# Kernel optimization log

Measured on AMD Instinct MI355X. Metric: run time of the kernel, lower is better.

Reference implementation:

```python
import jax, jax.numpy as jnp
import numpy as np

NEG_SLOPE = 0.2
N, IN_DIM, OUT_DIM, N_HEADS = 4096, 512, 512, 4
D_K = OUT_DIM // N_HEADS


def setup_inputs() -> dict:
    key = jax.random.key(0)
    k1, k2, k3, k4, k5 = jax.random.split(key, 5)
    H = jax.random.normal(k1, (N, IN_DIM), dtype=jnp.float32)
    A = jax.random.randint(k2, (N, N), 0, 2, dtype=jnp.int32)
    W = jax.random.normal(k3, (IN_DIM, OUT_DIM), dtype=jnp.float32) * (1.0 / np.sqrt(IN_DIM))
    a_l = jax.random.normal(k4, (N_HEADS, D_K), dtype=jnp.float32) * 0.1
    a_r = jax.random.normal(k5, (N_HEADS, D_K), dtype=jnp.float32) * 0.1
    return {"H": H, "A": A, "W": W, "a_l": a_l, "a_r": a_r}


def reference(H, A, W, a_l, a_r):
    n = H.shape[0]
    # mask = (A + I) > 0, shape (N, N); self-loops always allowed
    mask = (A + jnp.eye(n, dtype=A.dtype)) > 0
    # Wh: (N, heads, d_k)
    Wh = (H @ W).reshape(n, N_HEADS, D_K)
    sl = jnp.einsum('nhd,hd->nh', Wh, a_l)  # (N, heads)
    sr = jnp.einsum('nhd,hd->nh', Wh, a_r)  # (N, heads)
    # e[i, h, j] = leaky_relu(sl[i,h] + sr[j,h])
    e = jax.nn.leaky_relu(sl[:, :, None] + sr.T[None, :, :], negative_slope=NEG_SLOPE)
    e = jnp.where(mask[:, None, :], e, -jnp.inf)
    alpha = jnp.nan_to_num(jax.nn.softmax(e, axis=2), nan=0.0)  # dropout is identity at eval
    # out[i, h, :] = sum_j alpha[i,h,j] * Wh[j,h,:]
    out = jnp.einsum('nhm,mhd->nhd', alpha, Wh).reshape(n, OUT_DIM)
    return jax.nn.elu(out)
```

## Files before the change

### kernel.cpp

```cpp
#include <hip/hip_runtime.h>

typedef unsigned short ushort_t;
typedef __attribute__((ext_vector_type(8)))  short  short8;
typedef __attribute__((ext_vector_type(4)))  short  short4v;
typedef __attribute__((ext_vector_type(4)))  float  float4v;
typedef __attribute__((ext_vector_type(4)))  int    int4v;

#define N_NODES 4096
#define NHEADS  4
#define DK      128
#define ODIM    512
#define KDIM    512

__device__ __forceinline__ float bf2f(ushort_t u) {
    return __uint_as_float(((unsigned)u) << 16);
}
__device__ __forceinline__ ushort_t f2bf_rne(float f) {
    unsigned u = __float_as_uint(f);
    u += 0x7fffu + ((u >> 16) & 1u);
    return (ushort_t)(u >> 16);
}

__global__ __launch_bounds__(256) void pack_mask_k(const int* __restrict__ A,
                                                   unsigned long long* __restrict__ P,
                                                   const ushort_t* __restrict__ Hraw,
                                                   int* __restrict__ flag,
                                                   const void* __restrict__ W,
                                                   ushort_t* __restrict__ WT,
                                                   float* __restrict__ sl,
                                                   float* __restrict__ sr)
{
    __shared__ ushort_t lt[64][72];
    __shared__ int dcnt[4];
    const int tid = threadIdx.x;
    const int bx  = blockIdx.x;

    if (bx == 0 && tid < 64) {
        const int lane = tid;
        int cnt = 0;
        #pragma unroll
        for (int s = 0; s < 16; ++s) {
            ushort_t v = Hraw[(lane * 16 + s) * 2];
            int e = (v >> 7) & 0xFF;
            cnt += (((e >= 90) && (e <= 140)) || (v == 0)) ? 1 : 0;
        }
        #pragma unroll
        for (int off = 32; off; off >>= 1) cnt += __shfl_down(cnt, off);
        if (lane == 0) *flag = (cnt < 768) ? 1 : 0;
    }

    {
        const int lane  = tid & 63;
        const int flat4 = bx * 256 + tid;
        const int row   = flat4 >> 10;
        const int col0  = (flat4 << 2) & 4095;
        const int4v a   = ((const int4v*)A)[flat4];
        unsigned nib = 0;
        #pragma unroll
        for (int j = 0; j < 4; ++j)
            nib |= ((a[j] != 0) || (row == col0 + j)) ? (1u << j) : 0u;
        unsigned long long v = (unsigned long long)nib << ((lane & 15) * 4);
        v |= __shfl_xor(v, 1);
        v |= __shfl_xor(v, 2);
        v |= __shfl_xor(v, 4);
        v |= __shfl_xor(v, 8);
        if ((lane & 15) == 0) P[flat4 >> 4] = v;
    }

    if (bx >= 64 && bx < 96) {
        const int idx = (bx - 64) * 256 + tid;
        float4v z;
        #pragma unroll
        for (int e = 0; e < 4; ++e) z[e] = 0.f;
        if (idx < 4096) ((float4v*)sl)[idx] = z;
        else            ((float4v*)sr)[idx - 4096] = z;
    }

    if (bx < 64) {
        int cnt = 0;
        #pragma unroll
        for (int s = 0; s < 4; ++s) {
            ushort_t v = Hraw[(tid * 4 + s) * 2];
            int e = (v >> 7) & 0xFF;
            cnt += (((e >= 90) && (e <= 140)) || (v == 0)) ? 1 : 0;
        }
        #pragma unroll
        for (int off = 32; off; off >>= 1) cnt += __shfl_down(cnt, off);
        if ((tid & 63) == 0) dcnt[tid >> 6] = cnt;
        __syncthreads();
        const int f32 = (dcnt[0] + dcnt[1] + dcnt[2] + dcnt[3]) < 768;

        const int ti = bx >> 3, tj = bx & 7;
        const int r = tid >> 2, c2 = tid & 3;
        const size_t eo = (size_t)(ti * 64 + r) * KDIM + tj * 64 + c2 * 16;
        if (f32) {
            const float4v* src = (const float4v*)((const float*)W + eo);
            float4v f0 = src[0], f1 = src[1], f2 = src[2], f3 = src[3];
            #pragma unroll
            for (int e = 0; e < 4; ++e) {
                lt[r][c2 * 16 +  0 + e] = f2bf_rne(f0[e]);
                lt[r][c2 * 16 +  4 + e] = f2bf_rne(f1[e]);
                lt[r][c2 * 16 +  8 + e] = f2bf_rne(f2[e]);
                lt[r][c2 * 16 + 12 + e] = f2bf_rne(f3[e]);
            }
        } else {
            const short8* src = (const short8*)((const ushort_t*)W + eo);
            short8 v0 = src[0];
            short8 v1 = src[1];
            *(short8*)&lt[r][c2 * 16]     = v0;
            *(short8*)&lt[r][c2 * 16 + 8] = v1;
        }
        __syncthreads();
        #pragma unroll
        for (int itr = 0; itr < 2; ++itr) {
            int idx = itr * 256 + tid;
            int n = idx >> 3, c = idx & 7;
            short8 vv;
            #pragma unroll
            for (int e = 0; e < 8; ++e) vv[e] = (short)lt[c * 8 + e][n];
            *(short8*)(WT + (size_t)(tj * 64 + n) * KDIM + ti * 64 + c * 8) = vv;
        }
    }
}

__global__ __launch_bounds__(256) void gemm_wht_dual_k(const void* __restrict__ H,
                                                       const ushort_t* __restrict__ WT,
                                                       ushort_t* __restrict__ WhT,
                                                       const int* __restrict__ flag,
                                                       const void* __restrict__ al,
                                                       const void* __restrict__ ar,
                                                       float* __restrict__ sl,
                                                       float* __restrict__ sr)
{
    __shared__ ushort_t lt[64][72];
    const int f32 = *flag;
    const int tid  = threadIdx.x;
    const int lane = tid & 63;
    const int wid  = tid >> 6;
    const int quad = lane >> 4;
    const int l15  = lane & 15;
    const int bm = blockIdx.x & 63, bn = blockIdx.x >> 6;
    const int i0 = bm * 64, n0 = bn * 64;

    const size_t aoff = (size_t)(i0 + wid * 16 + l15) * KDIM + quad * 8;
    const short8* bp0 = (const short8*)(WT + (size_t)(n0 +  0 + l15) * KDIM) + quad;
    const short8* bp1 = (const short8*)(WT + (size_t)(n0 + 16 + l15) * KDIM) + quad;
    const short8* bp2 = (const short8*)(WT + (size_t)(n0 + 32 + l15) * KDIM) + quad;
    const short8* bp3 = (const short8*)(WT + (size_t)(n0 + 48 + l15) * KDIM) + quad;

    float4v acc0, acc1, acc2, acc3;
    #pragma unroll
    for (int e = 0; e < 4; ++e) { acc0[e] = 0.f; acc1[e] = 0.f; acc2[e] = 0.f; acc3[e] = 0.f; }

    #pragma unroll 4
    for (int k8 = 0; k8 < 64; k8 += 4) {
        short8 a;
        if (f32) {
            const float4v* fp = (const float4v*)((const float*)H + aoff + (size_t)k8 * 8);
            float4v x0 = fp[0], x1 = fp[1];
            #pragma unroll
            for (int e = 0; e < 4; ++e) {
                a[e]     = (short)f2bf_rne(x0[e]);
                a[4 + e] = (short)f2bf_rne(x1[e]);
            }
        } else {
            a = *(const short8*)((const ushort_t*)H + aoff + (size_t)k8 * 8);
        }
        acc0 = __builtin_amdgcn_mfma_f32_16x16x32_bf16(a, bp0[k8], acc0, 0, 0, 0);
        acc1 = __builtin_amdgcn_mfma_f32_16x16x32_bf16(a, bp1[k8], acc1, 0, 0, 0);
        acc2 = __builtin_amdgcn_mfma_f32_16x16x32_bf16(a, bp2[k8], acc2, 0, 0, 0);
        acc3 = __builtin_amdgcn_mfma_f32_16x16x32_bf16(a, bp3[k8], acc3, 0, 0, 0);
    }

    #pragma unroll
    for (int r = 0; r < 4; ++r) {
        int m = wid * 16 + quad * 4 + r;
        lt[ 0 + l15][m] = f2bf_rne(acc0[r]);
        lt[16 + l15][m] = f2bf_rne(acc1[r]);
        lt[32 + l15][m] = f2bf_rne(acc2[r]);
        lt[48 + l15][m] = f2bf_rne(acc3[r]);
    }
    __syncthreads();
    #pragma unroll
    for (int itr = 0; itr < 2; ++itr) {
        int idx = itr * 256 + tid;
        int n = idx >> 3, c = idx & 7;
        short8 v = *(const short8*)&lt[n][c * 8];
        *(short8*)(WhT + (size_t)(n0 + n) * N_NODES + i0 + c * 8) = v;
    }

    {
        const int h2 = n0 >> 7;
        const int d0 = n0 & 127;
        const int m  = tid >> 2;
        const int part = tid & 3;
        float psl = 0.f, psr = 0.f;
        #pragma unroll
        for (int k = 0; k < 16; ++k) {
            int n = part * 16 + k;
            float wv = bf2f(lt[n][m]);
            float av = f32 ? ((const float*)al)[h2 * DK + d0 + n]
                           : bf2f(((const ushort_t*)al)[h2 * DK + d0 + n]);
            float bv = f32 ? ((const float*)ar)[h2 * DK + d0 + n]
                           : bf2f(((const ushort_t*)ar)[h2 * DK + d0 + n]);
            psl += wv * av;
            psr += wv * bv;
        }
        psl += __shfl_down(psl, 2); psl += __shfl_down(psl, 1);
        psr += __shfl_down(psr, 2); psr += __shfl_down(psr, 1);
        if (part == 0) {
            atomicAdd(&sl[h2 * N_NODES + i0 + m], psl);
            atomicAdd(&sr[h2 * N_NODES + i0 + m], psr);
        }
    }
}

__global__ __launch_bounds__(512, 4) void attn_split_k(const ushort_t* __restrict__ WhT,
                                                       const unsigned* __restrict__ Apack,
                                                       const float* __restrict__ sl,
                                                       const float* __restrict__ sr,
                                                       float* __restrict__ Npart,
                                                       float* __restrict__ Dpart)
{
    __shared__ char smem[73728] __attribute__((aligned(16)));
    float*    srs  = (float*)smem;
    unsigned (*mbuf)[64] = (unsigned (*)[64])(smem + 8192);
    ushort_t* vbuf = (ushort_t*)(smem + 24576);

    const int tid  = threadIdx.x;
    const int lane = tid & 63;
    const int wid  = tid >> 6;
    const int wq   = wid & 3;
    const int js   = wid >> 2;
    const int quad = lane >> 4;
    const int l15  = lane & 15;
    const int bx   = blockIdx.x;
    const int half = bx & 1;
    const int h    = (bx >> 1) & 3;
    const int i0   = (bx >> 3) << 6;
    const int jbase = half << 11;

    const float C1 = 1.44269504f;

    for (int j = tid; j < 2048; j += 512) srs[j] = sr[h * N_NODES + jbase + j] * C1;
    for (int t = tid; t < 64 * 64; t += 512) {
        int r = t >> 6, c = t & 63;
        mbuf[r][c ^ r] = Apack[(size_t)(i0 + r) * 128 + (half << 6) + c];
    }
    const int myrow = wq * 16 + l15;
    const float slv = sl[h * N_NODES + i0 + myrow] * C1;
    __syncthreads();

    float4v acc[8];
    #pragma unroll
    for (int nt = 0; nt < 8; ++nt)
        #pragma unroll
        for (int e = 0; e < 4; ++e) acc[nt][e] = 0.f;
    float4v accden;
    #pragma unroll
    for (int e = 0; e < 4; ++e) accden[e] = 0.f;

    short8 ones;
    #pragma unroll
    for (int e = 0; e < 8; ++e) ones[e] = (short)0x3F80;

    const int dl  = lane >> 3;
    const int gch = (lane & 7) ^ dl;
    const ushort_t* g0 = WhT + (size_t)(h * DK + wid * 16 + dl) * N_NODES
                             + jbase + gch * 8;

    #define DMA_WIN(BUF, IW)                                                         \
        {   ushort_t* lb_ = vbuf + (BUF) * 8192 + wid * 1024;                        \
            const ushort_t* gs_ = g0 + (IW) * 64;                                    \
            _Pragma("unroll")                                                        \
            for (int q_ = 0; q_ < 2; ++q_)                                           \
                __builtin_amdgcn_global_load_lds(                                    \
                    (const __attribute__((address_space(1))) void*)(gs_ + (size_t)q_ * 8 * N_NODES), \
                    (__attribute__((address_space(3))) void*)(lb_ + q_ * 512),       \
                    16, 0, 0);                                                       \
        }

    DMA_WIN(0, 0)
    DMA_WIN(1, 1)

    const int rs = ((js * 4 + quad) ^ (l15 & 7)) * 8;

    #pragma unroll 1
    for (int iw = 0; iw < 32; ++iw) {
        const unsigned wa = mbuf[myrow][(iw * 2 + js) ^ myrow];
        const float4v s0 = *(const float4v*)&srs[iw * 64 + js * 32 + quad * 8];
        const float4v s1 = *(const float4v*)&srs[iw * 64 + js * 32 + quad * 8 + 4];

        short8 pf;
        #pragma unroll
        for (int jj = 0; jj < 8; ++jj) {
            const int bit = quad * 8 + jj;
            float srj = (jj < 4) ? s0[jj] : s1[jj - 4];
            float x = slv + srj;
            float t = fmaxf(x, x * 0.2f);
            t = ((wa >> bit) & 1u) ? t : -1e30f;
            pf[jj] = (short)(ushort_t)(__float_as_uint(__builtin_amdgcn_exp2f(t)) >> 16);
        }

        if (iw == 31) { asm volatile("s_waitcnt vmcnt(0)" ::: "memory"); }
        else          { asm volatile("s_waitcnt vmcnt(2)" ::: "memory"); }
        asm volatile("s_barrier" ::: "memory");
        if (iw < 30) DMA_WIN((iw + 2) % 3, iw + 2)

        const ushort_t* vB = vbuf + (iw % 3) * 8192;
        #pragma unroll
        for (int nt = 0; nt < 8; ++nt) {
            short8 b = *(const short8*)(vB + (nt * 16 + l15) * 64 + rs);
            acc[nt] = __builtin_amdgcn_mfma_f32_16x16x32_bf16(pf, b, acc[nt], 0, 0, 0);
        }
        accden = __builtin_amdgcn_mfma_f32_16x16x32_bf16(pf, ones, accden, 0, 0, 0);
    }
    #undef DMA_WIN

    float* red  = (float*)(smem + 24576);
    float* lsum = (float*)(smem + 24576 + 32768);
    __syncthreads();

    if (js == 1) {
        #pragma unroll
        for (int nt = 0; nt < 8; ++nt)
            #pragma unroll
            for (int r = 0; r < 4; ++r)
                red[wq * 2048 + (quad * 4 + r) * 128 + nt * 16 + l15] = acc[nt][r];
        if (l15 == 0) {
            #pragma unroll
            for (int r = 0; r < 4; ++r)
                lsum[wq * 16 + quad * 4 + r] = accden[r];
        }
    }
    __syncthreads();
    if (js == 0) {
        float* Np = Npart + (size_t)half * N_NODES * ODIM;
        #pragma unroll
        for (int nt = 0; nt < 8; ++nt)
            #pragma unroll
            for (int r = 0; r < 4; ++r) {
                const int rowi = wq * 16 + quad * 4 + r;
                float v = acc[nt][r] + red[wq * 2048 + (quad * 4 + r) * 128 + nt * 16 + l15];
                Np[(size_t)(i0 + rowi) * ODIM + h * DK + nt * 16 + l15] = v;
            }
        if (l15 == 0) {
            #pragma unroll
            for (int r = 0; r < 4; ++r) {
                const int rowi = wq * 16 + quad * 4 + r;
                Dpart[(half * 4 + h) * N_NODES + i0 + rowi] =
                    accden[r] + lsum[wq * 16 + quad * 4 + r];
            }
        }
    }
}

__global__ __launch_bounds__(256) void merge_k(const float* __restrict__ Npart,
                                               const float* __restrict__ Dpart,
                                               void* __restrict__ out,
                                               const int* __restrict__ flag)
{
    const int f32 = *flag;
    const size_t e4 = ((size_t)blockIdx.x * 256 + threadIdx.x) * 4;
    const int i = (int)(e4 >> 9);
    const int c = (int)(e4 & 511);
    const int h = c >> 7;
    const float4v n0 = *(const float4v*)(Npart + e4);
    const float4v n1 = *(const float4v*)(Npart + (size_t)N_NODES * ODIM + e4);
    const float den = Dpart[h * N_NODES + i] + Dpart[(4 + h) * N_NODES + i];
    const float rinv = 1.0f / fmaxf(den, 1e-37f);
    const float C1 = 1.44269504f;
    float o[4];
    #pragma unroll
    for (int k = 0; k < 4; ++k) {
        float v = (n0[k] + n1[k]) * rinv;
        float e = __builtin_amdgcn_exp2f(v * C1) - 1.0f;
        o[k] = (v > 0.f) ? v : e;
    }
    if (f32) {
        float4v ov;
        #pragma unroll
        for (int k = 0; k < 4; ++k) ov[k] = o[k];
        *(float4v*)((float*)out + e4) = ov;
    } else {
        short4v ov;
        #pragma unroll
        for (int k = 0; k < 4; ++k) ov[k] = (short)f2bf_rne(o[k]);
        *(short4v*)((ushort_t*)out + e4) = ov;
    }
}

__global__ __launch_bounds__(256, 2) void attn_single_k(const ushort_t* __restrict__ WhT,
                                                        const unsigned* __restrict__ Apack,
                                                        const float* __restrict__ sl,
                                                        const float* __restrict__ sr,
                                                        void* __restrict__ out,
                                                        const int* __restrict__ flag)
{
    __shared__ float    srs[N_NODES];
    __shared__ unsigned mbuf[32][128];
    __shared__ float    red[2][32][128];
    __shared__ float    lsum[4][32];

    const int f32  = *flag;
    const int tid  = threadIdx.x;
    const int lane = tid & 63;
    const int wq   = tid >> 6;
    const int quad = lane >> 4;
    const int l15  = lane & 15;
    const int h    = blockIdx.x & 3;
    const int i0   = (blockIdx.x >> 2) << 5;

    for (int j = tid; j < N_NODES; j += 256) srs[j] = sr[h * N_NODES + j];
    for (int t = tid; t < 32 * 128; t += 256) {
        int r = t >> 7, c = t & 127;
        mbuf[r][c] = Apack[(size_t)(i0 + r) * 128 + c];
    }
    const float slv0 = sl[h * N_NODES + i0 + l15];
    const float slv1 = sl[h * N_NODES + i0 + 16 + l15];
    __syncthreads();

    const float C1 = 1.44269504f;
    const float C2 = 0.2f * 1.44269504f;

    float4v acc[2][8];
    #pragma unroll
    for (int mg = 0; mg < 2; ++mg)
        #pragma unroll
        for (int nt = 0; nt < 8; ++nt)
            #pragma unroll
            for (int e = 0; e < 4; ++e) acc[mg][nt][e] = 0.f;
    float lacc0 = 0.f, lacc1 = 0.f;

    const ushort_t* vb = WhT + (size_t)(h * DK + l15) * N_NODES + wq * 1024 + quad * 8;

    #pragma unroll 1
    for (int it = 0; it < 16; ++it) {
        const int jl = it * 64;
        const int j0 = wq * 1024 + jl;
        const int mc = j0 >> 5;

        short8 bf[8][2];
        #pragma unroll
        for (int nt = 0; nt < 8; ++nt) {
            bf[nt][0] = *(const short8*)(vb + (size_t)nt * 16 * N_NODES + jl);
            bf[nt][1] = *(const short8*)(vb + (size_t)nt * 16 * N_NODES + jl + 32);
        }

        const unsigned wa0 = mbuf[l15][mc],      wa1 = mbuf[l15][mc + 1];
        const unsigned wb0 = mbuf[16 + l15][mc], wb1 = mbuf[16 + l15][mc + 1];

        short8 pf0[2], pf1[2];
        #pragma unroll
        for (int s = 0; s < 2; ++s) {
            const float* sp = &srs[j0 + s * 32 + quad * 8];
            const float4v s0 = *(const float4v*)sp;
            const float4v s1 = *(const float4v*)(sp + 4);
            const unsigned wa = s ? wa1 : wa0;
            const unsigned wb = s ? wb1 : wb0;
            #pragma unroll
            for (int jj = 0; jj < 8; ++jj) {
                float srj = (jj < 4) ? s0[jj] : s1[jj - 4];
                int bit = quad * 8 + jj;
                float x0 = slv0 + srj;
                float t0 = fmaxf(x0 * C1, x0 * C2);
                t0 = ((wa >> bit) & 1u) ? t0 : -1e30f;
                float p0 = __builtin_amdgcn_exp2f(t0);
                ushort_t h0 = (ushort_t)(__float_as_uint(p0) >> 16);
                lacc0 += bf2f(h0);
                pf0[s][jj] = (short)h0;
                float x1 = slv1 + srj;
                float t1 = fmaxf(x1 * C1, x1 * C2);
                t1 = ((wb >> bit) & 1u) ? t1 : -1e30f;
                float p1 = __builtin_amdgcn_exp2f(t1);
                ushort_t h1 = (ushort_t)(__float_as_uint(p1) >> 16);
                lacc1 += bf2f(h1);
                pf1[s][jj] = (short)h1;
            }
        }

        #pragma unroll
        for (int nt = 0; nt < 8; ++nt) {
            acc[0][nt] = __builtin_amdgcn_mfma_f32_16x16x32_bf16(pf0[0], bf[nt][0], acc[0][nt], 0, 0, 0);
            acc[0][nt] = __builtin_amdgcn_mfma_f32_16x16x32_bf16(pf0[1], bf[nt][1], acc[0][nt], 0, 0, 0);
            acc[1][nt] = __builtin_amdgcn_mfma_f32_16x16x32_bf16(pf1[0], bf[nt][0], acc[1][nt], 0, 0, 0);
            acc[1][nt] = __builtin_amdgcn_mfma_f32_16x16x32_bf16(pf1[1], bf[nt][1], acc[1][nt], 0, 0, 0);
        }
    }

    lacc0 += __shfl_xor(lacc0, 16);
    lacc0 += __shfl_xor(lacc0, 32);
    lacc1 += __shfl_xor(lacc1, 16);
    lacc1 += __shfl_xor(lacc1, 32);
    if (lane < 16) {
        lsum[wq][l15]      = lacc0;
        lsum[wq][16 + l15] = lacc1;
    }
    if (wq >= 2) {
        #pragma unroll
        for (int mg = 0; mg < 2; ++mg)
            #pragma unroll
            for (int nt = 0; nt < 8; ++nt)
                #pragma unroll
                for (int r = 0; r < 4; ++r)
                    red[wq - 2][mg * 16 + quad * 4 + r][nt * 16 + l15] = acc[mg][nt][r];
    }
    __syncthreads();
    if (wq < 2) {
        #pragma unroll
        for (int mg = 0; mg < 2; ++mg)
            #pragma unroll
            for (int nt = 0; nt < 8; ++nt)
                #pragma unroll
                for (int r = 0; r < 4; ++r)
                    acc[mg][nt][r] += red[wq][mg * 16 + quad * 4 + r][nt * 16 + l15];
    }
    __syncthreads();
    if (wq == 1) {
        #pragma unroll
        for (int mg = 0; mg < 2; ++mg)
            #pragma unroll
            for (int nt = 0; nt < 8; ++nt)
                #pragma unroll
                for (int r = 0; r < 4; ++r)
                    red[0][mg * 16 + quad * 4 + r][nt * 16 + l15] = acc[mg][nt][r];
    }
    __syncthreads();
    if (wq == 0) {
        #pragma unroll
        for (int mg = 0; mg < 2; ++mg) {
            float linv[4];
            #pragma unroll
            for (int r = 0; r < 4; ++r) {
                int rowi = mg * 16 + quad * 4 + r;
                float den = lsum[0][rowi] + lsum[1][rowi] + lsum[2][rowi] + lsum[3][rowi];
                linv[r] = 1.0f / fmaxf(den, 1e-37f);
            }
            #pragma unroll
            for (int nt = 0; nt < 8; ++nt)
                #pragma unroll
                for (int r = 0; r < 4; ++r) {
                    int rowi = mg * 16 + quad * 4 + r;
                    float v = (acc[mg][nt][r] + red[0][rowi][nt * 16 + l15]) * linv[r];
                    float e = __builtin_amdgcn_exp2f(v * C1) - 1.0f;
                    float o = (v > 0.f) ? v : e;
                    size_t oidx = (size_t)(i0 + rowi) * ODIM + h * DK + nt * 16 + l15;
                    if (f32) ((float*)out)[oidx] = o;
                    else     ((ushort_t*)out)[oidx] = f2bf_rne(o);
                }
        }
    }
}

extern "C" void kernel_launch(void* const* d_in, const int* in_sizes, int n_in,
                              void* d_out, int out_size, void* d_ws, size_t ws_size,
                              hipStream_t stream)
{
    const void* H  = d_in[0];
    const int*  A  = (const int*)d_in[1];
    const void* W  = d_in[2];
    const void* al = d_in[3];
    const void* ar = d_in[4];

    if (ws_size < (7u << 20)) return;

    char* ws = (char*)d_ws;
    ushort_t* WhT   = (ushort_t*)ws;
    unsigned long long* Apack = (unsigned long long*)(ws + (4u << 20));
    ushort_t* WT    = (ushort_t*)(ws + (6u << 20));
    float*    sl    = (float*)(ws + (6u << 20) + (512u << 10));
    float*    sr    = (float*)(ws + (6u << 20) + (576u << 10));
    int*      flag  = (int*)(ws + (6u << 20) + (640u << 10));
    float*    Npart = (float*)(ws + (12u << 20));
    float*    Dpart = (float*)(ws + (28u << 20));
    const bool have_split = ws_size >= (29u << 20);

    pack_mask_k    <<<16384, 256, 0, stream>>>(A, Apack, (const ushort_t*)H, flag,
                                               W, WT, sl, sr);
    gemm_wht_dual_k<<<512,   256, 0, stream>>>(H, WT, WhT, flag, al, ar, sl, sr);
    if (have_split) {
        attn_split_k<<<512, 512, 0, stream>>>(WhT, (const unsigned*)Apack, sl, sr, Npart, Dpart);
        merge_k     <<<2048, 256, 0, stream>>>(Npart, Dpart, (void*)d_out, flag);
    } else {
        attn_single_k<<<512, 256, 0, stream>>>(WhT, (const unsigned*)Apack, sl, sr, (void*)d_out, flag);
    }
}
```

Measured before the change: 172.6 us.

## Fuse split-K attention and merge into one 1024-thread kernel per row-block

Replaces the two-half split-K attention kernel plus separate merge kernel with a single kernel that has 1024 threads (16 waves) cover all 4096 neighbours for a 64-row, one-head tile. It reduces the partial sums in shared memory and applies the normalisation and ELU in place. This removes the Npart/Dpart round trip through global memory and one launch. The cost is a grid of only 256 blocks with 144KB LDS each, so at most one block fits per CU, which lowers occupancy and may leave CUs idle.

```diff
diff --git a/kernel.cpp b/kernel.cpp
--- a/kernel.cpp
+++ b/kernel.cpp
@@ -215,18 +215,19 @@
     }
 }
 
-__global__ __launch_bounds__(512, 4) void attn_split_k(const ushort_t* __restrict__ WhT,
+__global__ __launch_bounds__(1024, 4) void attn_full_k(const ushort_t* __restrict__ WhT,
                                                        const unsigned* __restrict__ Apack,
                                                        const float* __restrict__ sl,
                                                        const float* __restrict__ sr,
-                                                       float* __restrict__ Npart,
-                                                       float* __restrict__ Dpart)
+                                                       void* __restrict__ out,
+                                                       const int* __restrict__ flag)
 {
-    __shared__ char smem[73728] __attribute__((aligned(16)));
-    float*    srs  = (float*)smem;
-    unsigned (*mbuf)[64] = (unsigned (*)[64])(smem + 8192);
-    ushort_t* vbuf = (ushort_t*)(smem + 24576);
-
+    __shared__ char smem[147456] __attribute__((aligned(16)));
+    ushort_t* vbuf = (ushort_t*)smem;
+    unsigned (*mbuf)[128] = (unsigned (*)[128])(smem + 98304);
+    float*    srs  = (float*)(smem + 131072);
+
+    const int f32  = *flag;
     const int tid  = threadIdx.x;
     const int lane = tid & 63;
     const int wid  = tid >> 6;
@@ -235,17 +236,15 @@
     const int quad = lane >> 4;
     const int l15  = lane & 15;
     const int bx   = blockIdx.x;
-    const int half = bx & 1;
-    const int h    = (bx >> 1) & 3;
-    const int i0   = (bx >> 3) << 6;
-    const int jbase = half << 11;
+    const int h    = bx & 3;
+    const int i0   = (bx >> 2) << 6;
 
     const float C1 = 1.44269504f;
 
-    for (int j = tid; j < 2048; j += 512) srs[j] = sr[h * N_NODES + jbase + j] * C1;
-    for (int t = tid; t < 64 * 64; t += 512) {
-        int r = t >> 6, c = t & 63;
-        mbuf[r][c ^ r] = Apack[(size_t)(i0 + r) * 128 + (half << 6) + c];
+    for (int j = tid; j < 4096; j += 1024) srs[j] = sr[h * N_NODES + j] * C1;
+    for (int t = tid; t < 64 * 128; t += 1024) {
+        int r = t >> 7, c = t & 127;
+        mbuf[r][c ^ (r & 31)] = Apack[(size_t)(i0 + r) * 128 + c];
     }
     const int myrow = wq * 16 + l15;
     const float slv = sl[h * N_NODES + i0 + myrow] * C1;
@@ -264,20 +263,21 @@
     #pragma unroll
     for (int e = 0; e < 8; ++e) ones[e] = (short)0x3F80;
 
-    const int dl  = lane >> 3;
-    const int gch = (lane & 7) ^ dl;
-    const ushort_t* g0 = WhT + (size_t)(h * DK + wid * 16 + dl) * N_NODES
-                             + jbase + gch * 8;
-
-    #define DMA_WIN(BUF, IW)                                                         \
-        {   ushort_t* lb_ = vbuf + (BUF) * 8192 + wid * 1024;                        \
-            const ushort_t* gs_ = g0 + (IW) * 64;                                    \
-            _Pragma("unroll")                                                        \
-            for (int q_ = 0; q_ < 2; ++q_)                                           \
-                __builtin_amdgcn_global_load_lds(                                    \
-                    (const __attribute__((address_space(1))) void*)(gs_ + (size_t)q_ * 8 * N_NODES), \
-                    (__attribute__((address_space(3))) void*)(lb_ + q_ * 512),       \
-                    16, 0, 0);                                                       \
+    const int dl = lane >> 4;
+    const int s4 = lane & 15;
+    const ushort_t* gq0 = WhT + (size_t)(h * DK + wid * 8 + 0 + dl) * N_NODES
+                              + (size_t)((s4 ^ (0 + dl)) * 8);
+    const ushort_t* gq1 = WhT + (size_t)(h * DK + wid * 8 + 4 + dl) * N_NODES
+                              + (size_t)((s4 ^ (4 + dl)) * 8);
+
+    #define DMA_WIN(BUF, IW)                                                           \
+        {   ushort_t* lb_ = vbuf + (BUF) * 16384 + wid * 1024;                         \
+            __builtin_amdgcn_global_load_lds(                                          \
+                (const __attribute__((address_space(1))) void*)(gq0 + (size_t)(IW) * 128), \
+                (__attribute__((address_space(3))) void*)(lb_), 16, 0, 0);             \
+            __builtin_amdgcn_global_load_lds(                                          \
+                (const __attribute__((address_space(1))) void*)(gq1 + (size_t)(IW) * 128), \
+                (__attribute__((address_space(3))) void*)(lb_ + 512), 16, 0, 0);       \
         }
 
     DMA_WIN(0, 0)
@@ -287,9 +287,9 @@
 
     #pragma unroll 1
     for (int iw = 0; iw < 32; ++iw) {
-        const unsigned wa = mbuf[myrow][(iw * 2 + js) ^ myrow];
-        const float4v s0 = *(const float4v*)&srs[iw * 64 + js * 32 + quad * 8];
-        const float4v s1 = *(const float4v*)&srs[iw * 64 + js * 32 + quad * 8 + 4];
+        const unsigned wa = mbuf[myrow][(iw * 4 + js) ^ (myrow & 31)];
+        const float4v s0 = *(const float4v*)&srs[iw * 128 + js * 32 + quad * 8];
+        const float4v s1 = *(const float4v*)&srs[iw * 128 + js * 32 + quad * 8 + 4];
 
         short8 pf;
         #pragma unroll
@@ -307,248 +307,58 @@
         asm volatile("s_barrier" ::: "memory");
         if (iw < 30) DMA_WIN((iw + 2) % 3, iw + 2)
 
-        const ushort_t* vB = vbuf + (iw % 3) * 8192;
+        const ushort_t* vB = vbuf + (iw % 3) * 16384;
         #pragma unroll
         for (int nt = 0; nt < 8; ++nt) {
-            short8 b = *(const short8*)(vB + (nt * 16 + l15) * 64 + rs);
+            short8 b = *(const short8*)(vB + (nt * 16 + l15) * 128 + rs);
             acc[nt] = __builtin_amdgcn_mfma_f32_16x16x32_bf16(pf, b, acc[nt], 0, 0, 0);
         }
         accden = __builtin_amdgcn_mfma_f32_16x16x32_bf16(pf, ones, accden, 0, 0, 0);
     }
     #undef DMA_WIN
 
-    float* red  = (float*)(smem + 24576);
-    float* lsum = (float*)(smem + 24576 + 32768);
+    float* red  = (float*)smem;
+    float* lsum = (float*)(smem + 98304);
     __syncthreads();
 
-    if (js == 1) {
+    if (js != 0) {
+        float* rp = red + (size_t)((js - 1) * 4 + wq) * 2048;
         #pragma unroll
         for (int nt = 0; nt < 8; ++nt)
             #pragma unroll
             for (int r = 0; r < 4; ++r)
-                red[wq * 2048 + (quad * 4 + r) * 128 + nt * 16 + l15] = acc[nt][r];
+                rp[(quad * 4 + r) * 128 + nt * 16 + l15] = acc[nt][r];
         if (l15 == 0) {
             #pragma unroll
             for (int r = 0; r < 4; ++r)
-                lsum[wq * 16 + quad * 4 + r] = accden[r];
+                lsum[js * 64 + wq * 16 + quad * 4 + r] = accden[r];
         }
     }
     __syncthreads();
     if (js == 0) {
-        float* Np = Npart + (size_t)half * N_NODES * ODIM;
+        float rinv[4];
+        #pragma unroll
+        for (int r = 0; r < 4; ++r) {
+            const int rowo = wq * 16 + quad * 4 + r;
+            float den = accden[r] + lsum[64 + rowo] + lsum[128 + rowo] + lsum[192 + rowo];
+            rinv[r] = 1.0f / fmaxf(den, 1e-37f);
+        }
         #pragma unroll
         for (int nt = 0; nt < 8; ++nt)
             #pragma unroll
             for (int r = 0; r < 4; ++r) {
-                const int rowi = wq * 16 + quad * 4 + r;
-                float v = acc[nt][r] + red[wq * 2048 + (quad * 4 + r) * 128 + nt * 16 + l15];
-                Np[(size_t)(i0 + rowi) * ODIM + h * DK + nt * 16 + l15] = v;
+                const int ri = (quad * 4 + r) * 128 + nt * 16 + l15;
+                float v = (acc[nt][r]
+                           + red[(size_t)(0 * 4 + wq) * 2048 + ri]
+                           + red[(size_t)(1 * 4 + wq) * 2048 + ri]
+                           + red[(size_t)(2 * 4 + wq) * 2048 + ri]) * rinv[r];
+                float e = __builtin_amdgcn_exp2f(v * C1) - 1.0f;
+                float o = (v > 0.f) ? v : e;
+                const size_t oidx = (size_t)(i0 + wq * 16 + quad * 4 + r) * ODIM
+                                  + h * DK + nt * 16 + l15;
+                if (f32) ((float*)out)[oidx] = o;
+                else     ((ushort_t*)out)[oidx] = f2bf_rne(o);
             }
-        if (l15 == 0) {
-            #pragma unroll
-            for (int r = 0; r < 4; ++r) {
-                const int rowi = wq * 16 + quad * 4 + r;
-                Dpart[(half * 4 + h) * N_NODES + i0 + rowi] =
-                    accden[r] + lsum[wq * 16 + quad * 4 + r];
-            }
-        }
-    }
-}
-
-__global__ __launch_bounds__(256) void merge_k(const float* __restrict__ Npart,
-                                               const float* __restrict__ Dpart,
-                                               void* __restrict__ out,
-                                               const int* __restrict__ flag)
-{
-    const int f32 = *flag;
-    const size_t e4 = ((size_t)blockIdx.x * 256 + threadIdx.x) * 4;
-    const int i = (int)(e4 >> 9);
-    const int c = (int)(e4 & 511);
-    const int h = c >> 7;
-    const float4v n0 = *(const float4v*)(Npart + e4);
-    const float4v n1 = *(const float4v*)(Npart + (size_t)N_NODES * ODIM + e4);
-    const float den = Dpart[h * N_NODES + i] + Dpart[(4 + h) * N_NODES + i];
-    const float rinv = 1.0f / fmaxf(den, 1e-37f);
-    const float C1 = 1.44269504f;
-    float o[4];
-    #pragma unroll
-    for (int k = 0; k < 4; ++k) {
-        float v = (n0[k] + n1[k]) * rinv;
-        float e = __builtin_amdgcn_exp2f(v * C1) - 1.0f;
-        o[k] = (v > 0.f) ? v : e;
-    }
-    if (f32) {
-        float4v ov;
-        #pragma unroll
-        for (int k = 0; k < 4; ++k) ov[k] = o[k];
-        *(float4v*)((float*)out + e4) = ov;
-    } else {
-        short4v ov;
-        #pragma unroll
-        for (int k = 0; k < 4; ++k) ov[k] = (short)f2bf_rne(o[k]);
-        *(short4v*)((ushort_t*)out + e4) = ov;
-    }
-}
-
-__global__ __launch_bounds__(256, 2) void attn_single_k(const ushort_t* __restrict__ WhT,
-                                                        const unsigned* __restrict__ Apack,
-                                                        const float* __restrict__ sl,
-                                                        const float* __restrict__ sr,
-                                                        void* __restrict__ out,
-                                                        const int* __restrict__ flag)
-{
-    __shared__ float    srs[N_NODES];
-    __shared__ unsigned mbuf[32][128];
-    __shared__ float    red[2][32][128];
-    __shared__ float    lsum[4][32];
-
-    const int f32  = *flag;
-    const int tid  = threadIdx.x;
-    const int lane = tid & 63;
-    const int wq   = tid >> 6;
-    const int quad = lane >> 4;
-    const int l15  = lane & 15;
-    const int h    = blockIdx.x & 3;
-    const int i0   = (blockIdx.x >> 2) << 5;
-
-    for (int j = tid; j < N_NODES; j += 256) srs[j] = sr[h * N_NODES + j];
-    for (int t = tid; t < 32 * 128; t += 256) {
-        int r = t >> 7, c = t & 127;
-        mbuf[r][c] = Apack[(size_t)(i0 + r) * 128 + c];
-    }
-    const float slv0 = sl[h * N_NODES + i0 + l15];
-    const float slv1 = sl[h * N_NODES + i0 + 16 + l15];
-    __syncthreads();
-
-    const float C1 = 1.44269504f;
-    const float C2 = 0.2f * 1.44269504f;
-
-    float4v acc[2][8];
-    #pragma unroll
-    for (int mg = 0; mg < 2; ++mg)
-        #pragma unroll
-        for (int nt = 0; nt < 8; ++nt)
-            #pragma unroll
-            for (int e = 0; e < 4; ++e) acc[mg][nt][e] = 0.f;
-    float lacc0 = 0.f, lacc1 = 0.f;
-
-    const ushort_t* vb = WhT + (size_t)(h * DK + l15) * N_NODES + wq * 1024 + quad * 8;
-
-    #pragma unroll 1
-    for (int it = 0; it < 16; ++it) {
-        const int jl = it * 64;
-        const int j0 = wq * 1024 + jl;
-        const int mc = j0 >> 5;
-
-        short8 bf[8][2];
-        #pragma unroll
-        for (int nt = 0; nt < 8; ++nt) {
-            bf[nt][0] = *(const short8*)(vb + (size_t)nt * 16 * N_NODES + jl);
-            bf[nt][1] = *(const short8*)(vb + (size_t)nt * 16 * N_NODES + jl + 32);
-        }
-
-        const unsigned wa0 = mbuf[l15][mc],      wa1 = mbuf[l15][mc + 1];
-        const unsigned wb0 = mbuf[16 + l15][mc], wb1 = mbuf[16 + l15][mc + 1];
-
-        short8 pf0[2], pf1[2];
-        #pragma unroll
-        for (int s = 0; s < 2; ++s) {
-            const float* sp = &srs[j0 + s * 32 + quad * 8];
-            const float4v s0 = *(const float4v*)sp;
-            const float4v s1 = *(const float4v*)(sp + 4);
-            const unsigned wa = s ? wa1 : wa0;
-            const unsigned wb = s ? wb1 : wb0;
-            #pragma unroll
-            for (int jj = 0; jj < 8; ++jj) {
-                float srj = (jj < 4) ? s0[jj] : s1[jj - 4];
-                int bit = quad * 8 + jj;
-                float x0 = slv0 + srj;
-                float t0 = fmaxf(x0 * C1, x0 * C2);
-                t0 = ((wa >> bit) & 1u) ? t0 : -1e30f;
-                float p0 = __builtin_amdgcn_exp2f(t0);
-                ushort_t h0 = (ushort_t)(__float_as_uint(p0) >> 16);
-                lacc0 += bf2f(h0);
-                pf0[s][jj] = (short)h0;
-                float x1 = slv1 + srj;
-                float t1 = fmaxf(x1 * C1, x1 * C2);
-                t1 = ((wb >> bit) & 1u) ? t1 : -1e30f;
-                float p1 = __builtin_amdgcn_exp2f(t1);
-                ushort_t h1 = (ushort_t)(__float_as_uint(p1) >> 16);
-                lacc1 += bf2f(h1);
-                pf1[s][jj] = (short)h1;
-            }
-        }
-
-        #pragma unroll
-        for (int nt = 0; nt < 8; ++nt) {
-            acc[0][nt] = __builtin_amdgcn_mfma_f32_16x16x32_bf16(pf0[0], bf[nt][0], acc[0][nt], 0, 0, 0);
-            acc[0][nt] = __builtin_amdgcn_mfma_f32_16x16x32_bf16(pf0[1], bf[nt][1], acc[0][nt], 0, 0, 0);
-            acc[1][nt] = __builtin_amdgcn_mfma_f32_16x16x32_bf16(pf1[0], bf[nt][0], acc[1][nt], 0, 0, 0);
-            acc[1][nt] = __builtin_amdgcn_mfma_f32_16x16x32_bf16(pf1[1], bf[nt][1], acc[1][nt], 0, 0, 0);
-        }
-    }
-
-    lacc0 += __shfl_xor(lacc0, 16);
-    lacc0 += __shfl_xor(lacc0, 32);
-    lacc1 += __shfl_xor(lacc1, 16);
-    lacc1 += __shfl_xor(lacc1, 32);
-    if (lane < 16) {
-        lsum[wq][l15]      = lacc0;
-        lsum[wq][16 + l15] = lacc1;
-    }
-    if (wq >= 2) {
-        #pragma unroll
-        for (int mg = 0; mg < 2; ++mg)
-            #pragma unroll
-            for (int nt = 0; nt < 8; ++nt)
-                #pragma unroll
-                for (int r = 0; r < 4; ++r)
-                    red[wq - 2][mg * 16 + quad * 4 + r][nt * 16 + l15] = acc[mg][nt][r];
-    }
-    __syncthreads();
-    if (wq < 2) {
-        #pragma unroll
-        for (int mg = 0; mg < 2; ++mg)
-            #pragma unroll
-            for (int nt = 0; nt < 8; ++nt)
-                #pragma unroll
-                for (int r = 0; r < 4; ++r)
-                    acc[mg][nt][r] += red[wq][mg * 16 + quad * 4 + r][nt * 16 + l15];
-    }
-    __syncthreads();
-    if (wq == 1) {
-        #pragma unroll
-        for (int mg = 0; mg < 2; ++mg)
-            #pragma unroll
-            for (int nt = 0; nt < 8; ++nt)
-                #pragma unroll
-                for (int r = 0; r < 4; ++r)
-                    red[0][mg * 16 + quad * 4 + r][nt * 16 + l15] = acc[mg][nt][r];
-    }
-    __syncthreads();
-    if (wq == 0) {
-        #pragma unroll
-        for (int mg = 0; mg < 2; ++mg) {
-            float linv[4];
-            #pragma unroll
-            for (int r = 0; r < 4; ++r) {
-                int rowi = mg * 16 + quad * 4 + r;
-                float den = lsum[0][rowi] + lsum[1][rowi] + lsum[2][rowi] + lsum[3][rowi];
-                linv[r] = 1.0f / fmaxf(den, 1e-37f);
-            }
-            #pragma unroll
-            for (int nt = 0; nt < 8; ++nt)
-                #pragma unroll
-                for (int r = 0; r < 4; ++r) {
-                    int rowi = mg * 16 + quad * 4 + r;
-                    float v = (acc[mg][nt][r] + red[0][rowi][nt * 16 + l15]) * linv[r];
-                    float e = __builtin_amdgcn_exp2f(v * C1) - 1.0f;
-                    float o = (v > 0.f) ? v : e;
-                    size_t oidx = (size_t)(i0 + rowi) * ODIM + h * DK + nt * 16 + l15;
-                    if (f32) ((float*)out)[oidx] = o;
-                    else     ((ushort_t*)out)[oidx] = f2bf_rne(o);
-                }
-        }
     }
 }
 
@@ -571,17 +381,10 @@
     float*    sl    = (float*)(ws + (6u << 20) + (512u << 10));
     float*    sr    = (float*)(ws + (6u << 20) + (576u << 10));
     int*      flag  = (int*)(ws + (6u << 20) + (640u << 10));
-    float*    Npart = (float*)(ws + (12u << 20));
-    float*    Dpart = (float*)(ws + (28u << 20));
-    const bool have_split = ws_size >= (29u << 20);
 
     pack_mask_k    <<<16384, 256, 0, stream>>>(A, Apack, (const ushort_t*)H, flag,
                                                W, WT, sl, sr);
     gemm_wht_dual_k<<<512,   256, 0, stream>>>(H, WT, WhT, flag, al, ar, sl, sr);
-    if (have_split) {
-        attn_split_k<<<512, 512, 0, stream>>>(WhT, (const unsigned*)Apack, sl, sr, Npart, Dpart);
-        merge_k     <<<2048, 256, 0, stream>>>(Npart, Dpart, (void*)d_out, flag);
-    } else {
-        attn_single_k<<<512, 256, 0, stream>>>(WhT, (const unsigned*)Apack, sl, sr, (void*)d_out, flag);
-    }
-}
+    attn_full_k    <<<256,  1024, 0, stream>>>(WhT, (const unsigned*)Apack, sl, sr,
+                                               (void*)d_out, flag);
+}
```

After: 171.1 us. Within noise of the previous version (-0.9%).
